# Kernel tuning notes

Hardware: AMD Instinct MI355X
Metric: run time of the kernel (lower is better)

The kernel has to match this reference:

```python
import jax, jax.numpy as jnp
import numpy as np

N = 50000; E = 600000; D = 128; NB = 20; L = 3; H = 64; NG = 512; ZMAX = 100
CUTOFF = 5.0

def setup_inputs() -> dict:
    key = jax.random.key(0)
    ks = jax.random.split(key, 32)
    inp = {}
    inp['at_no'] = jax.random.randint(ks[0], (N,), 0, ZMAX)
    inp['pos'] = jax.random.normal(ks[1], (N, 3), dtype=jnp.float32) * 3.0
    inp['edge_index'] = jax.random.randint(ks[2], (2, E), 0, N)
    inp['batch'] = jnp.sort(jax.random.randint(ks[3], (N,), 0, NG))
    def w(k, shape, fan_in):
        return (jax.random.normal(k, shape, dtype=jnp.float32) / np.sqrt(fan_in)).astype(jnp.float32)
    inp['emb'] = w(ks[4], (ZMAX, D), 1.0)
    # per-block filter net: rbf -> 3D
    inp['Wf'] = w(ks[5], (L, NB, 3 * D), NB); inp['bf'] = jnp.zeros((L, 3 * D), jnp.float32)
    # per-block message scalar MLP: D -> D -> 3D
    inp['Wm1'] = w(ks[6], (L, D, D), D);      inp['bm1'] = jnp.zeros((L, D), jnp.float32)
    inp['Wm2'] = w(ks[7], (L, D, 3 * D), D);  inp['bm2'] = jnp.zeros((L, 3 * D), jnp.float32)
    # per-block update: U, V channel-mixing on vectors; MLP 2D -> D -> 3D
    inp['U'] = w(ks[8], (L, D, D), D)
    inp['V'] = w(ks[9], (L, D, D), D)
    inp['Wu1'] = w(ks[10], (L, 2 * D, D), 2 * D); inp['bu1'] = jnp.zeros((L, D), jnp.float32)
    inp['Wu2'] = w(ks[11], (L, D, 3 * D), D);     inp['bu2'] = jnp.zeros((L, 3 * D), jnp.float32)
    # scalar output head: D -> H -> 1, graph sum
    inp['Wo1'] = w(ks[12], (D, H), D); inp['bo1'] = jnp.zeros((H,), jnp.float32)
    inp['Wo2'] = w(ks[13], (H, 1), H); inp['bo2'] = jnp.zeros((1,), jnp.float32)
    return inp

def _painn(at_no, pos, edge_index, batch, emb, Wf, bf, Wm1, bm1, Wm2, bm2,
           U, V, Wu1, bu1, Wu2, bu2, Wo1, bo1, Wo2, bo2):
    src, dst = edge_index[0], edge_index[1]
    vec = pos[dst] - pos[src]                       # [E,3]
    dist = jnp.sqrt(jnp.sum(vec * vec, axis=-1, keepdims=True) + 1e-12)  # [E,1]
    dirv = vec / dist                               # [E,3] (rsh l=1)
    n = jnp.arange(1, NB + 1, dtype=jnp.float32)
    rbf = jnp.sin(n * jnp.pi * dist / CUTOFF) / dist            # [E,NB] Bessel
    fcut = 0.5 * (jnp.cos(jnp.pi * dist / CUTOFF) + 1.0) * (dist < CUTOFF)  # [E,1]

    x = emb[at_no]                                  # [N,D]
    v = jnp.zeros((x.shape[0], 3, D), x.dtype)      # [N,3,D]

    for l in range(L):
        # ---- message ----
        filt = (rbf @ Wf[l] + bf[l]) * fcut                     # [E,3D]
        phi = jax.nn.silu(x @ Wm1[l] + bm1[l]) @ Wm2[l] + bm2[l]  # [N,3D]
        m = phi[src] * filt                                     # [E,3D]
        ds, dv1, dv2 = m[:, :D], m[:, D:2 * D], m[:, 2 * D:]
        dv = dv1[:, None, :] * dirv[:, :, None] + dv2[:, None, :] * v[src]  # [E,3,D]
        x = x + jax.ops.segment_sum(ds, dst, num_segments=N)
        v = v + jax.ops.segment_sum(dv, dst, num_segments=N)
        # ---- update ----
        Uv = jnp.einsum('ncd,de->nce', v, U[l])
        Vv = jnp.einsum('ncd,de->nce', v, V[l])
        Vn = jnp.sqrt(jnp.sum(Vv * Vv, axis=1) + 1e-8)          # [N,D]
        a = jax.nn.silu(jnp.concatenate([x, Vn], axis=-1) @ Wu1[l] + bu1[l]) @ Wu2[l] + bu2[l]
        avv, asv, ass = a[:, :D], a[:, D:2 * D], a[:, 2 * D:]
        x = x + ass + asv * jnp.sum(Uv * Vv, axis=1)
        v = v + avv[:, None, :] * Uv

    node_out = jax.nn.silu(x @ Wo1 + bo1) @ Wo2 + bo2           # [N,1]
    return jax.ops.segment_sum(node_out, batch, num_segments=NG)  # [NG,1]

def reference(at_no, pos, edge_index, batch, emb, Wf, bf, Wm1, bm1, Wm2, bm2,
              U, V, Wu1, bu1, Wu2, bu2, Wo1, bo1, Wo2, bo2):
    return _painn(at_no, pos, edge_index, batch, emb, Wf, bf, Wm1, bm1, Wm2, bm2,
                  U, V, Wu1, bu1, Wu2, bu2, Wo1, bo1, Wo2, bo2)
```

## Files before the change

### kernel.cpp

```cpp
#include <hip/hip_runtime.h>
#include <math.h>

#define NN 50000
#define NE 600000
#define ECAP 230000
#define DD 128
#define D3 384
#define NB_ 20
#define HH 64
#define NG_ 512
#define LSZ 180224

typedef short v8s __attribute__((ext_vector_type(8)));
typedef short v4sh __attribute__((ext_vector_type(4)));
typedef float v4f __attribute__((ext_vector_type(4)));

__device__ __forceinline__ float silu_f(float z) { return z / (1.0f + expf(-z)); }

__device__ __forceinline__ short f2bf(float f) {
  unsigned u = __float_as_uint(f);
  u += 0x7FFF + ((u >> 16) & 1);
  return (short)(u >> 16);
}
__device__ __forceinline__ float bf2f(short s) {
  return __uint_as_float(((unsigned)(unsigned short)s) << 16);
}
__device__ __forceinline__ void split2(float x, short& h, short& l) {
  h = f2bf(x);
  l = f2bf(x - bf2f(h));
}
#define SPLIT8(f0, f1, ah, al) { short h,l; \
  split2(f0.x,h,l); ah[0]=h; al[0]=l;  split2(f0.y,h,l); ah[1]=h; al[1]=l; \
  split2(f0.z,h,l); ah[2]=h; al[2]=l;  split2(f0.w,h,l); ah[3]=h; al[3]=l; \
  split2(f1.x,h,l); ah[4]=h; al[4]=l;  split2(f1.y,h,l); ah[5]=h; al[5]=l; \
  split2(f1.z,h,l); ah[6]=h; al[6]=l;  split2(f1.w,h,l); ah[7]=h; al[7]=l; }
__device__ __forceinline__ void split_store4(float4 f, short* hp, short* lp) {
  short h0,l0,h1,l1,h2,l2,h3,l3;
  split2(f.x,h0,l0); split2(f.y,h1,l1); split2(f.z,h2,l2); split2(f.w,h3,l3);
  v4sh hv = {h0,h1,h2,h3}, lv = {l0,l1,l2,l3};
  *(v4sh*)hp = hv; *(v4sh*)lp = lv;
}
#define MFMA3(acc, ah, al, bh, bl) \
  acc = __builtin_amdgcn_mfma_f32_16x16x32_bf16(ah, bh, acc, 0, 0, 0); \
  acc = __builtin_amdgcn_mfma_f32_16x16x32_bf16(al, bh, acc, 0, 0, 0); \
  acc = __builtin_amdgcn_mfma_f32_16x16x32_bf16(ah, bl, acc, 0, 0, 0);

__global__ void zero_f_kernel(float* __restrict__ p, long n) {
  long i = (long)blockIdx.x * blockDim.x + threadIdx.x;
  long s = (long)gridDim.x * blockDim.x;
  for (; i < n; i += s) p[i] = 0.0f;
}

__global__ void zero_i_kernel(int* __restrict__ p, long n) {
  long i = (long)blockIdx.x * blockDim.x + threadIdx.x;
  long s = (long)gridDim.x * blockDim.x;
  for (; i < n; i += s) p[i] = 0;
}

__global__ void init_x_kernel(const int* __restrict__ at_no, const float* __restrict__ emb,
                              float* __restrict__ x) {
  int i = blockIdx.x * blockDim.x + threadIdx.x;
  if (i >= NN * DD) return;
  x[i] = emb[at_no[i >> 7] * DD + (i & 127)];
}

__global__ void prep_w_kernel(const float* __restrict__ Wm1, const float* __restrict__ Wm2,
                              const float* __restrict__ U, const float* __restrict__ V,
                              const float* __restrict__ Wu1, const float* __restrict__ Wu2,
                              short* __restrict__ hi, short* __restrict__ lo) {
  int idx = blockIdx.x * 256 + threadIdx.x;
  if (idx >= 3 * LSZ) return;
  int l = idx / LSZ, r = idx % LSZ;
  const float* src; int K, N, nk;
  if (r < 16384)       { src = Wm1 + (size_t)l*16384; K = 128; N = 128; nk = r; }
  else if (r < 65536)  { src = Wm2 + (size_t)l*49152; K = 128; N = 384; nk = r - 16384; }
  else if (r < 81920)  { src = U   + (size_t)l*16384; K = 128; N = 128; nk = r - 65536; }
  else if (r < 98304)  { src = V   + (size_t)l*16384; K = 128; N = 128; nk = r - 81920; }
  else if (r < 131072) { src = Wu1 + (size_t)l*32768; K = 256; N = 128; nk = r - 98304; }
  else                 { src = Wu2 + (size_t)l*49152; K = 128; N = 384; nk = r - 131072; }
  int n = nk / K, k = nk - n * K;
  float xx = src[(size_t)k * N + n];
  short h = f2bf(xx);
  hi[idx] = h;
  lo[idx] = f2bf(xx - bf2f(h));
}

__global__ void hist_kernel(const int* __restrict__ ei, const float* __restrict__ pos,
                            int* __restrict__ counts) {
  int e = blockIdx.x * blockDim.x + threadIdx.x;
  if (e >= NE) return;
  int s = ei[e], d = ei[NE + e];
  float dx = pos[3*d]   - pos[3*s];
  float dy = pos[3*d+1] - pos[3*s+1];
  float dz = pos[3*d+2] - pos[3*s+2];
  float d2 = dx*dx + dy*dy + dz*dz + 1e-12f;
  if (d2 < 25.0f) atomicAdd(&counts[d], 1);
}

__global__ void scan_kernel(const int* __restrict__ counts, int* __restrict__ indptr, int n) {
  __shared__ int sm[1024];
  __shared__ int carry_s;
  if (threadIdx.x == 0) carry_s = 0;
  __syncthreads();
  for (int start = 0; start < n; start += 1024) {
    int i = start + (int)threadIdx.x;
    int val = (i < n) ? counts[i] : 0;
    sm[threadIdx.x] = val;
    __syncthreads();
    for (int off = 1; off < 1024; off <<= 1) {
      int t = (threadIdx.x >= (unsigned)off) ? sm[threadIdx.x - off] : 0;
      __syncthreads();
      sm[threadIdx.x] += t;
      __syncthreads();
    }
    int c = carry_s;
    if (i < n) indptr[i] = c + sm[threadIdx.x] - val;
    __syncthreads();
    if (threadIdx.x == 0) carry_s = c + sm[1023];
    __syncthreads();
  }
  if (threadIdx.x == 0) indptr[n] = carry_s;
}

__global__ void fill_kernel(const int* __restrict__ ei, const float* __restrict__ pos,
                            const int* __restrict__ indptr, int* __restrict__ cursor,
                            int* __restrict__ srcs, float4* __restrict__ eg1,
                            float4* __restrict__ eg2) {
  int e = blockIdx.x * blockDim.x + threadIdx.x;
  if (e >= NE) return;
  int s = ei[e], d = ei[NE + e];
  float dx = pos[3*d]   - pos[3*s];
  float dy = pos[3*d+1] - pos[3*s+1];
  float dz = pos[3*d+2] - pos[3*s+2];
  float d2 = dx*dx + dy*dy + dz*dz + 1e-12f;
  if (d2 < 25.0f) {
    int p = atomicAdd(&cursor[d], 1);
    int slot = indptr[d] + p;
    float dist = sqrtf(d2);
    float inv = 1.0f / dist;
    float wang = 0.62831853071795864769f * dist;
    float s1 = __sinf(wang), c1 = __cosf(wang);
    float fc = 0.5f * (c1 + 1.0f);
    srcs[slot] = s;
    eg1[slot] = make_float4(s1, c1, fc, fc * inv);
    eg2[slot] = make_float4(dx * inv, dy * inv, dz * inv, 0.0f);
  }
}

template<bool SILU>
__global__ void __launch_bounds__(256) mfma_gemm_kernel(
    const float* A, const short* __restrict__ Bth, const short* __restrict__ Btl,
    const float* __restrict__ bias, float* C, int M) {
  __shared__ short As2[2 * 32 * 136];
  #define ASH(r,c) As2[(r)*136 + (c)]
  #define ASL(r,c) As2[4352 + (r)*136 + (c)]
  int tid = threadIdx.x;
  long r0 = (long)blockIdx.x * 32;
  #pragma unroll
  for (int i = 0; i < 4; i++) {
    int lin = i*256 + tid;
    int r = lin >> 5, c4 = lin & 31;
    long row = r0 + r; if (row >= M) row = M - 1;
    float4 f = *(const float4*)(A + row*128 + c4*4);
    split_store4(f, &ASH(r, c4*4), &ASL(r, c4*4));
  }
  __syncthreads();
  int lane = tid & 63, wv = tid >> 6;
  int l15 = lane & 15, q = lane >> 4;
  v4f acc[2][2] = {};
  #pragma unroll
  for (int s = 0; s < 4; s++) {
    v8s ah[2], al[2];
    #pragma unroll
    for (int mt = 0; mt < 2; mt++) {
      ah[mt] = *(const v8s*)&ASH(mt*16 + l15, s*32 + q*8);
      al[mt] = *(const v8s*)&ASL(mt*16 + l15, s*32 + q*8);
    }
    #pragma unroll
    for (int nt = 0; nt < 2; nt++) {
      int n = (2*wv + nt)*16 + l15;
      v8s bh = *(const v8s*)(Bth + (long)n*128 + s*32 + q*8);
      v8s bl = *(const v8s*)(Btl + (long)n*128 + s*32 + q*8);
      #pragma unroll
      for (int mt = 0; mt < 2; mt++) { MFMA3(acc[mt][nt], ah[mt], al[mt], bh, bl); }
    }
  }
  #pragma unroll
  for (int nt = 0; nt < 2; nt++) {
    int n = (2*wv + nt)*16 + l15;
    float bb = bias[n];
    #pragma unroll
    for (int mt = 0; mt < 2; mt++)
      #pragma unroll
      for (int i = 0; i < 4; i++) {
        long row = r0 + mt*16 + q*4 + i;
        if (row < M) {
          float val = acc[mt][nt][i] + bb;
          if constexpr (SILU) val = silu_f(val);
          C[row*128 + n] = val;
        }
      }
  }
  #undef ASH
  #undef ASL
}

__global__ void __launch_bounds__(512) mfma_gemm_phi_kernel(
    const float* A, const short* __restrict__ Bth, const short* __restrict__ Btl,
    const float* __restrict__ bias,
    float* __restrict__ C0, float* __restrict__ C1, float* C2, int M) {
  __shared__ short As2[2 * 32 * 136];
  #define ASH(r,c) As2[(r)*136 + (c)]
  #define ASL(r,c) As2[4352 + (r)*136 + (c)]
  int tid = threadIdx.x;
  long r0 = (long)blockIdx.x * 32;
  #pragma unroll
  for (int i = 0; i < 2; i++) {
    int lin = i*512 + tid;
    int r = lin >> 5, c4 = lin & 31;
    long row = r0 + r; if (row >= M) row = M - 1;
    float4 f = *(const float4*)(A + row*128 + c4*4);
    split_store4(f, &ASH(r, c4*4), &ASL(r, c4*4));
  }
  __syncthreads();
  int lane = tid & 63, wv = tid >> 6;
  int l15 = lane & 15, q = lane >> 4;
  v4f acc[2][3] = {};
  #pragma unroll
  for (int s = 0; s < 4; s++) {
    v8s ah[2], al[2];
    #pragma unroll
    for (int mt = 0; mt < 2; mt++) {
      ah[mt] = *(const v8s*)&ASH(mt*16 + l15, s*32 + q*8);
      al[mt] = *(const v8s*)&ASL(mt*16 + l15, s*32 + q*8);
    }
    #pragma unroll
    for (int j = 0; j < 3; j++) {
      int n = (wv*3 + j)*16 + l15;
      v8s bh = *(const v8s*)(Bth + (long)n*128 + s*32 + q*8);
      v8s bl = *(const v8s*)(Btl + (long)n*128 + s*32 + q*8);
      #pragma unroll
      for (int mt = 0; mt < 2; mt++) { MFMA3(acc[mt][j], ah[mt], al[mt], bh, bl); }
    }
  }
  #pragma unroll
  for (int j = 0; j < 3; j++) {
    int n = (wv*3 + j)*16 + l15;
    int sl = n >> 7, col = n & 127;
    float* C = (sl == 0) ? C0 : (sl == 1) ? C1 : C2;
    float bb = bias[n];
    #pragma unroll
    for (int mt = 0; mt < 2; mt++)
      #pragma unroll
      for (int i = 0; i < 4; i++) {
        long row = r0 + mt*16 + q*4 + i;
        if (row < M) C[row*128 + col] = acc[mt][j][i] + bb;
      }
  }
  #undef ASH
  #undef ASL
}

__global__ void __launch_bounds__(512) muva_kernel(
    const float* __restrict__ phi0, const float* __restrict__ phi1,
    const float* __restrict__ phi2, const float* __restrict__ vA,
    float* __restrict__ vB, float* __restrict__ x,
    const int* __restrict__ srcs, const float4* __restrict__ eg1,
    const float4* __restrict__ eg2, const int* __restrict__ indptr,
    const float* __restrict__ Wf_l, const float* __restrict__ bf_l,
    const short* __restrict__ Uth, const short* __restrict__ Utl,
    const short* __restrict__ Vth, const short* __restrict__ Vtl,
    const short* __restrict__ W1h, const short* __restrict__ W1l, const float* __restrict__ b1,
    const short* __restrict__ W2h, const short* __restrict__ W2l, const float* __restrict__ b2) {
  __shared__ float smem[8896];
  #define VN(r,c)  smem[(r)*140 + (c)]
  #define XN(r,c)  smem[6720 + (r)*136 + (c)]
  #define CAT(r,c) smem[(r)*276 + (c)]
  #define T2(r,c)  smem[4416 + (r)*140 + (c)]
  const long NND = (long)NN*DD;
  int tid = threadIdx.x;
  long nb = (long)blockIdx.x * 16;
  {
    int g = tid >> 7, d = tid & 127;
    float wf0[NB_], wf1[NB_], wf2[NB_];
    #pragma unroll
    for (int k = 0; k < NB_; k++) {
      wf0[k] = Wf_l[k*D3 + d];
      wf1[k] = Wf_l[k*D3 + DD + d];
      wf2[k] = Wf_l[k*D3 + 2*DD + d];
    }
    float bf0 = bf_l[d], bf1 = bf_l[DD + d], bf2 = bf_l[2*DD + d];
    for (int j = 0; j < 4; j++) {
      int nr = 4*g + j;
      long n = nb + nr;
      int t = indptr[n], end = indptr[n+1];
      float xacc = 0.f, a0 = 0.f, a1 = 0.f, a2 = 0.f;
      float4 g1C = {}, g2C = {};
      float p0C = 0.f, p1C = 0.f, p2C = 0.f, w0C = 0.f, w1C = 0.f, w2C = 0.f;
      if (t < end) {
        int s0 = srcs[t]; g1C = eg1[t]; g2C = eg2[t];
        long b = (long)s0*DD + d;
        p0C = phi0[b]; p1C = phi1[b]; p2C = phi2[b];
        w0C = vA[b]; w1C = vA[NND + b]; w2C = vA[2*NND + b];
      }
      for (; t < end; t++) {
        float4 gg = g1C, dv = g2C;
        float p0 = p0C, p1 = p1C, p2 = p2C, w0 = w0C, w1 = w1C, w2 = w2C;
        if (t + 1 < end) {
          int sN = srcs[t+1]; g1C = eg1[t+1]; g2C = eg2[t+1];
          long b = (long)sN*DD + d;
          p0C = phi0[b]; p1C = phi1[b]; p2C = phi2[b];
          w0C = vA[b]; w1C = vA[NND + b]; w2C = vA[2*NND + b];
        }
        float c2 = 2.0f * gg.y;
        float rkm1 = 0.f, rk = gg.x, dot0 = 0.f, dot1 = 0.f, dot2 = 0.f;
        #pragma unroll
        for (int k = 0; k < NB_; k++) {
          dot0 = fmaf(rk, wf0[k], dot0);
          dot1 = fmaf(rk, wf1[k], dot1);
          dot2 = fmaf(rk, wf2[k], dot2);
          float rn = fmaf(c2, rk, -rkm1);
          rkm1 = rk; rk = rn;
        }
        xacc = fmaf(p0, bf0*gg.z + gg.w*dot0, xacc);
        float m1 = p1 * (bf1*gg.z + gg.w*dot1);
        float m2 = p2 * (bf2*gg.z + gg.w*dot2);
        a0 = fmaf(m1, dv.x, fmaf(m2, w0, a0));
        a1 = fmaf(m1, dv.y, fmaf(m2, w1, a1));
        a2 = fmaf(m1, dv.z, fmaf(m2, w2, a2));
      }
      long b = n*DD + d;
      XN(nr, d) = x[b] + xacc;
      VN(nr, d)      = vA[b]         + a0;
      VN(16 + nr, d) = vA[NND + b]   + a1;
      VN(32 + nr, d) = vA[2*NND + b] + a2;
    }
  }
  __syncthreads();
  int lane = tid & 63, wv = tid >> 6;
  int l15 = lane & 15, q = lane >> 4;
  int d = wv*16 + l15;
  v4f aU[3] = {}, aV[3] = {};
  #pragma unroll
  for (int s = 0; s < 4; s++) {
    long boff = (long)d*128 + s*32 + q*8;
    v8s buh = *(const v8s*)(Uth + boff);
    v8s bul = *(const v8s*)(Utl + boff);
    v8s bvh = *(const v8s*)(Vth + boff);
    v8s bvl = *(const v8s*)(Vtl + boff);
    #pragma unroll
    for (int c = 0; c < 3; c++) {
      float4 f0 = *(const float4*)&VN(c*16 + l15, s*32 + q*8);
      float4 f1 = *(const float4*)&VN(c*16 + l15, s*32 + q*8 + 4);
      v8s ah, al;
      SPLIT8(f0, f1, ah, al);
      MFMA3(aU[c], ah, al, buh, bul);
      MFMA3(aV[c], ah, al, bvh, bvl);
    }
  }
  float sreg[4], vn2[4];
  #pragma unroll
  for (int i = 0; i < 4; i++) {
    sreg[i] = aU[0][i]*aV[0][i] + aU[1][i]*aV[1][i] + aU[2][i]*aV[2][i];
    vn2[i]  = aV[0][i]*aV[0][i] + aV[1][i]*aV[1][i] + aV[2][i]*aV[2][i];
  }
  float vold[4][3];
  #pragma unroll
  for (int i = 0; i < 4; i++)
    #pragma unroll
    for (int c = 0; c < 3; c++) vold[i][c] = VN(c*16 + q*4 + i, d);
  __syncthreads();
  {
    int r = tid >> 5, c4 = tid & 31;
    *(float4*)&CAT(r, c4*4) = *(const float4*)&XN(r, c4*4);
  }
  #pragma unroll
  for (int i = 0; i < 4; i++)
    CAT(q*4 + i, 128 + d) = sqrtf(vn2[i] + 1e-8f);
  __syncthreads();
  {
    v4f acc = {};
    #pragma unroll
    for (int s = 0; s < 8; s++) {
      float4 f0 = *(const float4*)&CAT(l15, s*32 + q*8);
      float4 f1 = *(const float4*)&CAT(l15, s*32 + q*8 + 4);
      v8s ah, al;
      SPLIT8(f0, f1, ah, al);
      v8s bh = *(const v8s*)(W1h + (long)d*256 + s*32 + q*8);
      v8s bl = *(const v8s*)(W1l + (long)d*256 + s*32 + q*8);
      MFMA3(acc, ah, al, bh, bl);
    }
    float bb = b1[d];
    #pragma unroll
    for (int i = 0; i < 4; i++)
      T2(q*4 + i, d) = silu_f(acc[i] + bb);
  }
  __syncthreads();
  {
    v4f acc[3] = {};
    #pragma unroll
    for (int s = 0; s < 4; s++) {
      float4 f0 = *(const float4*)&T2(l15, s*32 + q*8);
      float4 f1 = *(const float4*)&T2(l15, s*32 + q*8 + 4);
      v8s ah, al;
      SPLIT8(f0, f1, ah, al);
      #pragma unroll
      for (int g = 0; g < 3; g++) {
        int n = g*128 + d;
        v8s bh = *(const v8s*)(W2h + (long)n*128 + s*32 + q*8);
        v8s bl = *(const v8s*)(W2l + (long)n*128 + s*32 + q*8);
        MFMA3(acc[g], ah, al, bh, bl);
      }
    }
    float bavv = b2[d], basv = b2[128 + d], bass = b2[256 + d];
    #pragma unroll
    for (int i = 0; i < 4; i++) {
      int lr = q*4 + i;
      long row = nb + lr;
      float avv = acc[0][i] + bavv;
      float asv = acc[1][i] + basv;
      float ass = acc[2][i] + bass;
      x[row*DD + d] = CAT(lr, d) + ass + asv * sreg[i];
      #pragma unroll
      for (int c = 0; c < 3; c++)
        vB[(long)c*NND + row*DD + d] = fmaf(avv, aU[c][i], vold[i][c]);
    }
  }
  #undef VN
  #undef XN
  #undef CAT
  #undef T2
}

__global__ void __launch_bounds__(256) out_kernel(
    const float* __restrict__ x, const float* __restrict__ Wo1,
    const float* __restrict__ bo1, const float* __restrict__ Wo2,
    const float* __restrict__ bo2, const int* __restrict__ batch,
    float* __restrict__ out) {
  __shared__ float xs[4][132];
  int tid = threadIdx.x;
  long n0 = (long)blockIdx.x * 4;
  if (tid < 128) {
    int r = tid >> 5, c4 = tid & 31;
    *(float4*)&xs[r][c4*4] = *(const float4*)(x + (n0 + r)*128 + c4*4);
  }
  __syncthreads();
  int wv = tid >> 6, t = tid & 63;
  float acc = bo1[t];
  #pragma unroll 16
  for (int k = 0; k < DD; k++) acc = fmaf(xs[wv][k], Wo1[k*HH + t], acc);
  float val = silu_f(acc) * Wo2[t];
  #pragma unroll
  for (int off = 32; off > 0; off >>= 1) val += __shfl_down(val, off);
  if (t == 0) atomicAdd(&out[batch[n0 + wv]], val + bo2[0]);
}

extern "C" void kernel_launch(void* const* d_in, const int* in_sizes, int n_in,
                              void* d_out, int out_size, void* d_ws, size_t ws_size,
                              hipStream_t stream) {
  const int*   at_no = (const int*)d_in[0];
  const float* pos   = (const float*)d_in[1];
  const int*   ei    = (const int*)d_in[2];
  const int*   batch = (const int*)d_in[3];
  const float* emb   = (const float*)d_in[4];
  const float* Wf    = (const float*)d_in[5];
  const float* bfp   = (const float*)d_in[6];
  const float* Wm1   = (const float*)d_in[7];
  const float* bm1   = (const float*)d_in[8];
  const float* Wm2   = (const float*)d_in[9];
  const float* bm2   = (const float*)d_in[10];
  const float* U     = (const float*)d_in[11];
  const float* V     = (const float*)d_in[12];
  const float* Wu1   = (const float*)d_in[13];
  const float* bu1   = (const float*)d_in[14];
  const float* Wu2   = (const float*)d_in[15];
  const float* bu2   = (const float*)d_in[16];
  const float* Wo1   = (const float*)d_in[17];
  const float* bo1   = (const float*)d_in[18];
  const float* Wo2   = (const float*)d_in[19];
  const float* bo2   = (const float*)d_in[20];
  float* out = (float*)d_out;

  char* w = (char*)d_ws;
  auto alloc = [&](size_t bytes) -> void* {
    void* p = (void*)w;
    w += (bytes + 255) & ~(size_t)255;
    return p;
  };
  float*  x      = (float*)alloc(sizeof(float)*(size_t)NN*DD);
  float*  v_a    = (float*)alloc(sizeof(float)*(size_t)NN*D3);
  float*  v_b    = (float*)alloc(sizeof(float)*(size_t)NN*D3);
  float*  t1     = (float*)alloc(sizeof(float)*(size_t)NN*DD);
  float*  phiS   = (float*)alloc(sizeof(float)*(size_t)NN*DD);
  float*  phi0   = (float*)alloc(sizeof(float)*(size_t)NN*DD);
  short*  wbh    = (short*)alloc(sizeof(short)*(size_t)3*LSZ);
  short*  wbl    = (short*)alloc(sizeof(short)*(size_t)3*LSZ);
  int*    srcs   = (int*)alloc(sizeof(int)*(size_t)ECAP);
  float4* eg1    = (float4*)alloc(sizeof(float4)*(size_t)ECAP);
  float4* eg2    = (float4*)alloc(sizeof(float4)*(size_t)ECAP);
  int*    indptr = (int*)alloc(sizeof(int)*((size_t)NN+1));
  int*    counts = (int*)alloc(sizeof(int)*(size_t)NN);

  if ((size_t)(w - (char*)d_ws) > ws_size) {
    zero_f_kernel<<<2, 256, 0, stream>>>(out, NG_);
    return;
  }

  zero_f_kernel<<<2048, 256, 0, stream>>>(v_a, (long)NN*D3);
  zero_f_kernel<<<2, 256, 0, stream>>>(out, NG_);
  zero_i_kernel<<<64, 256, 0, stream>>>(counts, NN);
  init_x_kernel<<<(NN*DD + 255)/256, 256, 0, stream>>>(at_no, emb, x);
  prep_w_kernel<<<(3*LSZ + 255)/256, 256, 0, stream>>>(Wm1, Wm2, U, V, Wu1, Wu2, wbh, wbl);
  hist_kernel<<<(NE + 255)/256, 256, 0, stream>>>(ei, pos, counts);
  scan_kernel<<<1, 1024, 0, stream>>>(counts, indptr, NN);
  zero_i_kernel<<<64, 256, 0, stream>>>(counts, NN);
  fill_kernel<<<(NE + 255)/256, 256, 0, stream>>>(ei, pos, indptr, counts, srcs, eg1, eg2);

  const int MB = (NN + 31) / 32;
  float* vcur = v_a;
  float* vnext = v_b;
  for (int l = 0; l < 3; l++) {
    const float* Wf_l  = Wf  + (size_t)l*NB_*D3;
    const float* bf_l  = bfp + (size_t)l*D3;
    const float* bm1_l = bm1 + (size_t)l*DD;
    const float* bm2_l = bm2 + (size_t)l*D3;
    const float* bu1_l = bu1 + (size_t)l*DD;
    const float* bu2_l = bu2 + (size_t)l*D3;
    const short* Lh = wbh + (size_t)l*LSZ;
    const short* Ll = wbl + (size_t)l*LSZ;
    const short* Wm1h = Lh,          *Wm1L = Ll;
    const short* Wm2h = Lh + 16384,  *Wm2L = Ll + 16384;
    const short* Uh   = Lh + 65536,  *UL   = Ll + 65536;
    const short* Vh   = Lh + 81920,  *VL   = Ll + 81920;
    const short* Wu1h = Lh + 98304,  *Wu1L = Ll + 98304;
    const short* Wu2h = Lh + 131072, *Wu2L = Ll + 131072;

    mfma_gemm_kernel<true><<<MB, 256, 0, stream>>>(x, Wm1h, Wm1L, bm1_l, t1, NN);
    mfma_gemm_phi_kernel<<<MB, 512, 0, stream>>>(t1, Wm2h, Wm2L, bm2_l, phi0, phiS, t1, NN);
    muva_kernel<<<NN/16, 512, 0, stream>>>(phi0, phiS, t1, vcur, vnext, x,
                                           srcs, eg1, eg2, indptr, Wf_l, bf_l,
                                           Uh, UL, Vh, VL,
                                           Wu1h, Wu1L, bu1_l, Wu2h, Wu2L, bu2_l);

    float* tmp = vcur; vcur = vnext; vnext = tmp;
  }

  out_kernel<<<NN/4, 256, 0, stream>>>(x, Wo1, bo1, Wo2, bo2, batch, out);

  (void)in_sizes; (void)n_in; (void)out_size; (void)ws_size;
}
```

Before: 1.472 ms.

## Fuse message MLP GEMMs and store pre-split bf16 operands in LDS

Fuses the two message-MLP GEMMs into one kernel, so the silu hidden layer stays in shared memory as pre-split hi/lo bf16 and is never written to or reread from global memory. In the update kernel, activations are split into hi/lo bf16 once when written to LDS instead of at every MFMA operand load. It also balances the edge-aggregation work across the four wave groups using prefix sums of edge counts instead of fixed four-node chunks. The cost is more LDS per block and some extra barriers. vold is now rebuilt from hi+lo, so it is close to the original fp32 value but not exactly equal.

```diff
diff --git a/kernel.cpp b/kernel.cpp
--- a/kernel.cpp
+++ b/kernel.cpp
@@ -29,11 +29,6 @@
   h = f2bf(x);
   l = f2bf(x - bf2f(h));
 }
-#define SPLIT8(f0, f1, ah, al) { short h,l; \
-  split2(f0.x,h,l); ah[0]=h; al[0]=l;  split2(f0.y,h,l); ah[1]=h; al[1]=l; \
-  split2(f0.z,h,l); ah[2]=h; al[2]=l;  split2(f0.w,h,l); ah[3]=h; al[3]=l; \
-  split2(f1.x,h,l); ah[4]=h; al[4]=l;  split2(f1.y,h,l); ah[5]=h; al[5]=l; \
-  split2(f1.z,h,l); ah[6]=h; al[6]=l;  split2(f1.w,h,l); ah[7]=h; al[7]=l; }
 __device__ __forceinline__ void split_store4(float4 f, short* hp, short* lp) {
   short h0,l0,h1,l1,h2,l2,h3,l3;
   split2(f.x,h0,l0); split2(f.y,h1,l1); split2(f.z,h2,l2); split2(f.w,h3,l3);
@@ -147,71 +142,16 @@
   }
 }
 
-template<bool SILU>
-__global__ void __launch_bounds__(256) mfma_gemm_kernel(
-    const float* A, const short* __restrict__ Bth, const short* __restrict__ Btl,
-    const float* __restrict__ bias, float* C, int M) {
-  __shared__ short As2[2 * 32 * 136];
-  #define ASH(r,c) As2[(r)*136 + (c)]
-  #define ASL(r,c) As2[4352 + (r)*136 + (c)]
-  int tid = threadIdx.x;
-  long r0 = (long)blockIdx.x * 32;
-  #pragma unroll
-  for (int i = 0; i < 4; i++) {
-    int lin = i*256 + tid;
-    int r = lin >> 5, c4 = lin & 31;
-    long row = r0 + r; if (row >= M) row = M - 1;
-    float4 f = *(const float4*)(A + row*128 + c4*4);
-    split_store4(f, &ASH(r, c4*4), &ASL(r, c4*4));
-  }
-  __syncthreads();
-  int lane = tid & 63, wv = tid >> 6;
-  int l15 = lane & 15, q = lane >> 4;
-  v4f acc[2][2] = {};
-  #pragma unroll
-  for (int s = 0; s < 4; s++) {
-    v8s ah[2], al[2];
-    #pragma unroll
-    for (int mt = 0; mt < 2; mt++) {
-      ah[mt] = *(const v8s*)&ASH(mt*16 + l15, s*32 + q*8);
-      al[mt] = *(const v8s*)&ASL(mt*16 + l15, s*32 + q*8);
-    }
-    #pragma unroll
-    for (int nt = 0; nt < 2; nt++) {
-      int n = (2*wv + nt)*16 + l15;
-      v8s bh = *(const v8s*)(Bth + (long)n*128 + s*32 + q*8);
-      v8s bl = *(const v8s*)(Btl + (long)n*128 + s*32 + q*8);
-      #pragma unroll
-      for (int mt = 0; mt < 2; mt++) { MFMA3(acc[mt][nt], ah[mt], al[mt], bh, bl); }
-    }
-  }
-  #pragma unroll
-  for (int nt = 0; nt < 2; nt++) {
-    int n = (2*wv + nt)*16 + l15;
-    float bb = bias[n];
-    #pragma unroll
-    for (int mt = 0; mt < 2; mt++)
-      #pragma unroll
-      for (int i = 0; i < 4; i++) {
-        long row = r0 + mt*16 + q*4 + i;
-        if (row < M) {
-          float val = acc[mt][nt][i] + bb;
-          if constexpr (SILU) val = silu_f(val);
-          C[row*128 + n] = val;
-        }
-      }
-  }
-  #undef ASH
-  #undef ASL
-}
-
-__global__ void __launch_bounds__(512) mfma_gemm_phi_kernel(
-    const float* A, const short* __restrict__ Bth, const short* __restrict__ Btl,
-    const float* __restrict__ bias,
-    float* __restrict__ C0, float* __restrict__ C1, float* C2, int M) {
-  __shared__ short As2[2 * 32 * 136];
-  #define ASH(r,c) As2[(r)*136 + (c)]
-  #define ASL(r,c) As2[4352 + (r)*136 + (c)]
+__global__ void __launch_bounds__(512) mlp_phi_kernel(
+    const float* __restrict__ x,
+    const short* __restrict__ W1h, const short* __restrict__ W1l, const float* __restrict__ b1,
+    const short* __restrict__ W2h, const short* __restrict__ W2l, const float* __restrict__ b2,
+    float* __restrict__ C0, float* __restrict__ C1, float* __restrict__ C2, int M) {
+  __shared__ short sm[4 * 32 * 136];
+  #define XH_(r,c) sm[(r)*136 + (c)]
+  #define XL_(r,c) sm[4352 + (r)*136 + (c)]
+  #define TH_(r,c) sm[8704 + (r)*136 + (c)]
+  #define TL_(r,c) sm[13056 + (r)*136 + (c)]
   int tid = threadIdx.x;
   long r0 = (long)blockIdx.x * 32;
   #pragma unroll
@@ -219,26 +159,52 @@
     int lin = i*512 + tid;
     int r = lin >> 5, c4 = lin & 31;
     long row = r0 + r; if (row >= M) row = M - 1;
-    float4 f = *(const float4*)(A + row*128 + c4*4);
-    split_store4(f, &ASH(r, c4*4), &ASL(r, c4*4));
+    float4 f = *(const float4*)(x + row*128 + c4*4);
+    split_store4(f, &XH_(r, c4*4), &XL_(r, c4*4));
   }
   __syncthreads();
   int lane = tid & 63, wv = tid >> 6;
   int l15 = lane & 15, q = lane >> 4;
+  {
+    int n = wv*16 + l15;
+    v4f acc[2] = {};
+    #pragma unroll
+    for (int s = 0; s < 4; s++) {
+      v8s bh = *(const v8s*)(W1h + (long)n*128 + s*32 + q*8);
+      v8s bl = *(const v8s*)(W1l + (long)n*128 + s*32 + q*8);
+      #pragma unroll
+      for (int mt = 0; mt < 2; mt++) {
+        v8s ah = *(const v8s*)&XH_(mt*16 + l15, s*32 + q*8);
+        v8s al = *(const v8s*)&XL_(mt*16 + l15, s*32 + q*8);
+        MFMA3(acc[mt], ah, al, bh, bl);
+      }
+    }
+    float bb = b1[n];
+    #pragma unroll
+    for (int mt = 0; mt < 2; mt++)
+      #pragma unroll
+      for (int i = 0; i < 4; i++) {
+        short h, l;
+        split2(silu_f(acc[mt][i] + bb), h, l);
+        TH_(mt*16 + q*4 + i, n) = h;
+        TL_(mt*16 + q*4 + i, n) = l;
+      }
+  }
+  __syncthreads();
   v4f acc[2][3] = {};
   #pragma unroll
   for (int s = 0; s < 4; s++) {
     v8s ah[2], al[2];
     #pragma unroll
     for (int mt = 0; mt < 2; mt++) {
-      ah[mt] = *(const v8s*)&ASH(mt*16 + l15, s*32 + q*8);
-      al[mt] = *(const v8s*)&ASL(mt*16 + l15, s*32 + q*8);
+      ah[mt] = *(const v8s*)&TH_(mt*16 + l15, s*32 + q*8);
+      al[mt] = *(const v8s*)&TL_(mt*16 + l15, s*32 + q*8);
     }
     #pragma unroll
     for (int j = 0; j < 3; j++) {
       int n = (wv*3 + j)*16 + l15;
-      v8s bh = *(const v8s*)(Bth + (long)n*128 + s*32 + q*8);
-      v8s bl = *(const v8s*)(Btl + (long)n*128 + s*32 + q*8);
+      v8s bh = *(const v8s*)(W2h + (long)n*128 + s*32 + q*8);
+      v8s bl = *(const v8s*)(W2l + (long)n*128 + s*32 + q*8);
       #pragma unroll
       for (int mt = 0; mt < 2; mt++) { MFMA3(acc[mt][j], ah[mt], al[mt], bh, bl); }
     }
@@ -248,7 +214,7 @@
     int n = (wv*3 + j)*16 + l15;
     int sl = n >> 7, col = n & 127;
     float* C = (sl == 0) ? C0 : (sl == 1) ? C1 : C2;
-    float bb = bias[n];
+    float bb = b2[n];
     #pragma unroll
     for (int mt = 0; mt < 2; mt++)
       #pragma unroll
@@ -257,8 +223,10 @@
         if (row < M) C[row*128 + col] = acc[mt][j][i] + bb;
       }
   }
-  #undef ASH
-  #undef ASL
+  #undef XH_
+  #undef XL_
+  #undef TH_
+  #undef TL_
 }
 
 __global__ void __launch_bounds__(512) muva_kernel(
@@ -272,14 +240,32 @@
     const short* __restrict__ Vth, const short* __restrict__ Vtl,
     const short* __restrict__ W1h, const short* __restrict__ W1l, const float* __restrict__ b1,
     const short* __restrict__ W2h, const short* __restrict__ W2l, const float* __restrict__ b2) {
-  __shared__ float smem[8896];
-  #define VN(r,c)  smem[(r)*140 + (c)]
-  #define XN(r,c)  smem[6720 + (r)*136 + (c)]
-  #define CAT(r,c) smem[(r)*276 + (c)]
-  #define T2(r,c)  smem[4416 + (r)*140 + (c)]
+  __shared__ short svn[13056];
+  __shared__ float xnf[16*136];
+  __shared__ int bnd[5];
+  #define VNH(r,c)  svn[(r)*136 + (c)]
+  #define VNL(r,c)  svn[6528 + (r)*136 + (c)]
+  #define CATH(r,c) svn[(r)*264 + (c)]
+  #define CATL(r,c) svn[4224 + (r)*264 + (c)]
+  #define T2H(r,c)  svn[8448 + (r)*136 + (c)]
+  #define T2L(r,c)  svn[10624 + (r)*136 + (c)]
+  #define XN(r,c)   xnf[(r)*136 + (c)]
   const long NND = (long)NN*DD;
   int tid = threadIdx.x;
   long nb = (long)blockIdx.x * 16;
+  if (tid == 0) {
+    int base = indptr[nb];
+    int tot = indptr[nb + 16] - base;
+    bnd[0] = 0;
+    int g = 1;
+    for (int i = 1; i <= 16 && g < 4; i++) {
+      int pre = indptr[nb + i] - base;
+      while (g < 4 && 4*pre >= g*tot) bnd[g++] = i;
+    }
+    while (g < 4) bnd[g++] = 16;
+    bnd[4] = 16;
+  }
+  __syncthreads();
   {
     int g = tid >> 7, d = tid & 127;
     float wf0[NB_], wf1[NB_], wf2[NB_];
@@ -290,8 +276,7 @@
       wf2[k] = Wf_l[k*D3 + 2*DD + d];
     }
     float bf0 = bf_l[d], bf1 = bf_l[DD + d], bf2 = bf_l[2*DD + d];
-    for (int j = 0; j < 4; j++) {
-      int nr = 4*g + j;
+    for (int nr = bnd[g]; nr < bnd[g+1]; nr++) {
       long n = nb + nr;
       int t = indptr[n], end = indptr[n+1];
       float xacc = 0.f, a0 = 0.f, a1 = 0.f, a2 = 0.f;
@@ -331,9 +316,10 @@
       }
       long b = n*DD + d;
       XN(nr, d) = x[b] + xacc;
-      VN(nr, d)      = vA[b]         + a0;
-      VN(16 + nr, d) = vA[NND + b]   + a1;
-      VN(32 + nr, d) = vA[2*NND + b] + a2;
+      short h, l;
+      split2(vA[b] + a0, h, l);          VNH(nr, d) = h;      VNL(nr, d) = l;
+      split2(vA[NND + b] + a1, h, l);    VNH(16+nr, d) = h;   VNL(16+nr, d) = l;
+      split2(vA[2*NND + b] + a2, h, l);  VNH(32+nr, d) = h;   VNL(32+nr, d) = l;
     }
   }
   __syncthreads();
@@ -350,10 +336,8 @@
     v8s bvl = *(const v8s*)(Vtl + boff);
     #pragma unroll
     for (int c = 0; c < 3; c++) {
-      float4 f0 = *(const float4*)&VN(c*16 + l15, s*32 + q*8);
-      float4 f1 = *(const float4*)&VN(c*16 + l15, s*32 + q*8 + 4);
-      v8s ah, al;
-      SPLIT8(f0, f1, ah, al);
+      v8s ah = *(const v8s*)&VNH(c*16 + l15, s*32 + q*8);
+      v8s al = *(const v8s*)&VNL(c*16 + l15, s*32 + q*8);
       MFMA3(aU[c], ah, al, buh, bul);
       MFMA3(aV[c], ah, al, bvh, bvl);
     }
@@ -368,42 +352,48 @@
   #pragma unroll
   for (int i = 0; i < 4; i++)
     #pragma unroll
-    for (int c = 0; c < 3; c++) vold[i][c] = VN(c*16 + q*4 + i, d);
+    for (int c = 0; c < 3; c++)
+      vold[i][c] = bf2f(VNH(c*16 + q*4 + i, d)) + bf2f(VNL(c*16 + q*4 + i, d));
   __syncthreads();
   {
     int r = tid >> 5, c4 = tid & 31;
-    *(float4*)&CAT(r, c4*4) = *(const float4*)&XN(r, c4*4);
-  }
-  #pragma unroll
-  for (int i = 0; i < 4; i++)
-    CAT(q*4 + i, 128 + d) = sqrtf(vn2[i] + 1e-8f);
+    float4 f = *(const float4*)&XN(r, c4*4);
+    split_store4(f, &CATH(r, c4*4), &CATL(r, c4*4));
+  }
+  #pragma unroll
+  for (int i = 0; i < 4; i++) {
+    short h, l;
+    split2(sqrtf(vn2[i] + 1e-8f), h, l);
+    CATH(q*4 + i, 128 + d) = h;
+    CATL(q*4 + i, 128 + d) = l;
+  }
   __syncthreads();
   {
     v4f acc = {};
     #pragma unroll
     for (int s = 0; s < 8; s++) {
-      float4 f0 = *(const float4*)&CAT(l15, s*32 + q*8);
-      float4 f1 = *(const float4*)&CAT(l15, s*32 + q*8 + 4);
-      v8s ah, al;
-      SPLIT8(f0, f1, ah, al);
+      v8s ah = *(const v8s*)&CATH(l15, s*32 + q*8);
+      v8s al = *(const v8s*)&CATL(l15, s*32 + q*8);
       v8s bh = *(const v8s*)(W1h + (long)d*256 + s*32 + q*8);
       v8s bl = *(const v8s*)(W1l + (long)d*256 + s*32 + q*8);
       MFMA3(acc, ah, al, bh, bl);
     }
     float bb = b1[d];
     #pragma unroll
-    for (int i = 0; i < 4; i++)
-      T2(q*4 + i, d) = silu_f(acc[i] + bb);
+    for (int i = 0; i < 4; i++) {
+      short h, l;
+      split2(silu_f(acc[i] + bb), h, l);
+      T2H(q*4 + i, d) = h;
+      T2L(q*4 + i, d) = l;
+    }
   }
   __syncthreads();
   {
     v4f acc[3] = {};
     #pragma unroll
     for (int s = 0; s < 4; s++) {
-      float4 f0 = *(const float4*)&T2(l15, s*32 + q*8);
-      float4 f1 = *(const float4*)&T2(l15, s*32 + q*8 + 4);
-      v8s ah, al;
-      SPLIT8(f0, f1, ah, al);
+      v8s ah = *(const v8s*)&T2H(l15, s*32 + q*8);
+      v8s al = *(const v8s*)&T2L(l15, s*32 + q*8);
       #pragma unroll
       for (int g = 0; g < 3; g++) {
         int n = g*128 + d;
@@ -420,16 +410,19 @@
       float avv = acc[0][i] + bavv;
       float asv = acc[1][i] + basv;
       float ass = acc[2][i] + bass;
-      x[row*DD + d] = CAT(lr, d) + ass + asv * sreg[i];
+      x[row*DD + d] = XN(lr, d) + ass + asv * sreg[i];
       #pragma unroll
       for (int c = 0; c < 3; c++)
         vB[(long)c*NND + row*DD + d] = fmaf(avv, aU[c][i], vold[i][c]);
     }
   }
-  #undef VN
+  #undef VNH
+  #undef VNL
+  #undef CATH
+  #undef CATL
+  #undef T2H
+  #undef T2L
   #undef XN
-  #undef CAT
-  #undef T2
 }
 
 __global__ void __launch_bounds__(256) out_kernel(
@@ -535,8 +528,8 @@
     const short* Wu1h = Lh + 98304,  *Wu1L = Ll + 98304;
     const short* Wu2h = Lh + 131072, *Wu2L = Ll + 131072;
 
-    mfma_gemm_kernel<true><<<MB, 256, 0, stream>>>(x, Wm1h, Wm1L, bm1_l, t1, NN);
-    mfma_gemm_phi_kernel<<<MB, 512, 0, stream>>>(t1, Wm2h, Wm2L, bm2_l, phi0, phiS, t1, NN);
+    mlp_phi_kernel<<<MB, 512, 0, stream>>>(x, Wm1h, Wm1L, bm1_l, Wm2h, Wm2L, bm2_l,
+                                           phi0, phiS, t1, NN);
     muva_kernel<<<NN/16, 512, 0, stream>>>(phi0, phiS, t1, vcur, vnext, x,
                                            srcs, eg1, eg2, indptr, Wf_l, bf_l,
                                            Uh, UL, Vh, VL,
```

New measurement: 1.491 ms. Within noise of the previous version (+1.3%).
